# Optimization experiments

Hardware: AMD Instinct MI355X
Metric: run time of the kernel (lower is better)

## Reference

```python
import jax, jax.numpy as jnp
import numpy as np

H = 1024
T = 50000
WASHOUT = 200
SPECTRAL_RADIUS = 0.9


def setup_inputs() -> dict:
    key = jax.random.key(0)
    k_u, k_in, k_res, k_mask = jax.random.split(key, 4)
    u = jax.random.normal(k_u, (T,), dtype=jnp.float32)
    # w_in ~ Uniform(-0.5, 0.5), density 1.0, input_scaling 1.0
    w_in = jax.random.uniform(k_in, (H,), dtype=jnp.float32) - 0.5
    # w_res ~ Uniform(-0.5, 0.5), density 1.0, scaled to spectral radius 0.9
    w_res = np.asarray(jax.random.uniform(k_res, (H, H), dtype=jnp.float32)) - 0.5
    rho = float(np.max(np.abs(np.linalg.eigvals(w_res.astype(np.float64)))))
    w_res = jnp.asarray((SPECTRAL_RADIUS / rho) * w_res, dtype=jnp.float32)
    # readout weights (inference path uses the buffer, initialized to ones)
    w_out = jnp.ones((H,), dtype=jnp.float32)
    # w_out_density = 1.0 -> mask is a random permutation of all H indices
    w_out_mask = jax.random.permutation(k_mask, H).astype(jnp.int64)
    return {"u": u, "w_in": w_in, "w_res": w_res, "w_out": w_out,
            "w_out_mask": w_out_mask}


def reference(u, w_in, w_res, w_out, w_out_mask):
    # Echo-state recurrence: x_t = tanh(w_in * u_t + w_res @ x_{t-1})
    # Inference path (y=None, awgn_test_std=0, adc_quantization=None).
    def step(x, u_t):
        x_new = jnp.tanh(w_in * u_t + w_res @ x)  # [H]
        return x_new, x_new[w_out_mask]           # emit masked state

    x0 = jnp.zeros((H,), dtype=u.dtype)
    _, X = jax.lax.scan(step, x0, u)              # X: [T, H]
    return X[WASHOUT:] @ w_out                    # [T - WASHOUT]
```

## Files before the change

kernel.cpp:

```cpp
#include <hip/hip_runtime.h>


#define HH    1024
#define TT    50000
#define WASH  200
#define NBROLE 32
#define NBLK  512
#define NT    256
#define SPIN_CAP (1u << 20)
#define LDSPAD 98304

typedef unsigned int u32;
typedef u32 u32x4 __attribute__((ext_vector_type(4)));
typedef float f32x4 __attribute__((ext_vector_type(4)));
typedef float f32x2 __attribute__((ext_vector_type(2)));

__device__ __forceinline__ float fast_tanh(float x) {
  float e = __builtin_amdgcn_exp2f(x * 2.8853900817779268f);
  return fmaf(-2.0f, __builtin_amdgcn_rcpf(e + 1.0f), 1.0f);
}

template <int CTRL>
__device__ __forceinline__ float dpp_movf(float x) {
  return __int_as_float(__builtin_amdgcn_update_dpp(
      0, __float_as_int(x), CTRL, 0xF, 0xF, true));
}
__device__ __forceinline__ float swz_xor16(float x) {
  return __int_as_float(__builtin_amdgcn_ds_swizzle(__float_as_int(x), 0x401F));
}

#define YREDUCE()                                                         \
  { y += __shfl_xor(y, 32);                                               \
    y += swz_xor16(y);                                                    \
    y += dpp_movf<0x128>(y);                             \
    y += dpp_movf<0x141>(y);                             \
    y += dpp_movf<0x1B>(y);                              \
    y += dpp_movf<0xB1>(y); }

#define POLL_ISSUE1(b)                                                    \
  asm volatile("global_load_dwordx4 %0, %1, off sc1" : "=v"(p) : "v"(b))
#define POLL_WAIT1()                                                      \
  asm volatile("s_waitcnt vmcnt(0)" : "+v"(p))

#define TAGBAD(q) ((((q.x ^ want) | (q.y ^ want) | (q.z ^ want) | (q.w ^ want)) & 0xFFu))

#define UNPACK2(q, b2)                                                    \
  { xv2[b2+0] = (f32x2){__uint_as_float(q.x & 0xFFFFFF00u),               \
                        __uint_as_float(q.y & 0xFFFFFF00u)};              \
    xv2[b2+1] = (f32x2){__uint_as_float(q.z & 0xFFFFFF00u),               \
                        __uint_as_float(q.w & 0xFFFFFF00u)}; }

#define DECLW(r) f32x2 W##r##0, W##r##1, W##r##2, W##r##3,                \
                      W##r##4, W##r##5, W##r##6, W##r##7

#define LOADW(r) do {                                                     \
  const float* wp = w_res + (size_t)(32 * b + 8 * ww + r) * HH + 4 * l;   \
  f32x4 va = *(const f32x4*)(wp);                                         \
  f32x4 vb = *(const f32x4*)(wp + 256);                                   \
  f32x4 vc = *(const f32x4*)(wp + 512);                                   \
  f32x4 vd = *(const f32x4*)(wp + 768);                                   \
  W##r##0 = (f32x2){va.x, va.y}; W##r##1 = (f32x2){va.z, va.w};           \
  W##r##2 = (f32x2){vb.x, vb.y}; W##r##3 = (f32x2){vb.z, vb.w};           \
  W##r##4 = (f32x2){vc.x, vc.y}; W##r##5 = (f32x2){vc.z, vc.w};           \
  W##r##6 = (f32x2){vd.x, vd.y}; W##r##7 = (f32x2){vd.z, vd.w};           \
} while (0)

#define FMAR(r) do {                                                      \
  acc2[r] = __builtin_elementwise_fma(W##r##0, xv2[0], acc2[r]);          \
  acc2[r] = __builtin_elementwise_fma(W##r##1, xv2[1], acc2[r]);          \
  acc2[r] = __builtin_elementwise_fma(W##r##2, xv2[2], acc2[r]);          \
  acc2[r] = __builtin_elementwise_fma(W##r##3, xv2[3], acc2[r]);          \
  acc2[r] = __builtin_elementwise_fma(W##r##4, xv2[4], acc2[r]);          \
  acc2[r] = __builtin_elementwise_fma(W##r##5, xv2[5], acc2[r]);          \
  acc2[r] = __builtin_elementwise_fma(W##r##6, xv2[6], acc2[r]);          \
  acc2[r] = __builtin_elementwise_fma(W##r##7, xv2[7], acc2[r]);          \
} while (0)

__global__ __launch_bounds__(NT, 1) void esn_kernel(
    const float* __restrict__ u,
    const float* __restrict__ w_in,
    const float* __restrict__ w_res,
    const float* __restrict__ w_out,
    const int*   __restrict__ mask,
    float*       __restrict__ out,
    char*        __restrict__ ws)
{
  const int tid = threadIdx.x;
  const int l  = tid & 63;
  const int ww = tid >> 6;

  u32 xcc;
  asm("s_getreg_b32 %0, hwreg(HW_REG_XCC_ID)" : "=s"(xcc));
  if (xcc != 0) return;

  __shared__ __align__(16) char lds_all[LDSPAD];
  float* lds_c = (float*)lds_all;
  u32 (*lds_x)[HH] = (u32 (*)[HH])(lds_all + 4096);
  int* slot_p = (int*)(lds_all + 4096 + 8192);

  if (tid == 0) *slot_p = atomicAdd((int*)ws, 1);
  for (int h = tid; h < HH; h += NT) lds_c[mask[h]] = w_out[h];
  __syncthreads();
  const int b = *slot_p;
  if (b >= NBROLE) return;

  u32* xb0 = (u32*)(ws + 4096);
  u32* xb1 = xb0 + HH;

  DECLW(0); DECLW(1); DECLW(2); DECLW(3);
  DECLW(4); DECLW(5); DECLW(6); DECLW(7);
  LOADW(0); LOADW(1); LOADW(2); LOADW(3);
  LOADW(4); LOADW(5); LOADW(6); LOADW(7);

  const float win = w_in[32 * b + 8 * ww + (l >> 3)];

  f32x2 cr2[8];
#pragma unroll
  for (int k = 0; k < 4; ++k) {
    f32x4 v = *(const f32x4*)(lds_c + 256 * k + 4 * l);
    cr2[2*k+0] = (f32x2){v.x, v.y};
    cr2[2*k+1] = (f32x2){v.z, v.w};
  }

  const u32* pS0 = xb0 + 256 * ww + 4 * l;
  const u32* pS1 = xb1 + 256 * ww + 4 * l;
  const int drow = 32 * b + 8 * ww + (l >> 3);
  u32* d0 = xb0 + drow;
  u32* d1 = xb1 + drow;
  const int stg = 256 * ww + 4 * l;

  const int role = (b << 2) | ww;
  u32x4 p;
  const int lb32 = l & 32, lb16 = l & 16, lb8 = l & 8;
  int dead = 0;

  for (int t = 0; t < TT; ++t) {
    const int pa = t & 1;
    const float u_t = u[t];
    f32x2 acc2[8];
#pragma unroll
    for (int i = 0; i < 8; ++i) acc2[i] = (f32x2){0.f, 0.f};
    f32x2 xv2[8];
    const bool doRead = ((t & 127) == role) && (t > 0);

    if (t > 0) {
      const int h = pa ^ 1;
      if (!dead) {
        __builtin_amdgcn_s_sleep(2);
        const u32* src = h ? pS1 : pS0;
        const u32 want = (u32)t & 0xFFu;
        u32 guard = 0;
        for (;;) {
          POLL_ISSUE1(src);
          POLL_WAIT1();
          if (!TAGBAD(p)) break;
          if (++guard > SPIN_CAP) { dead = 1; break; }
        }
      }
      *(u32x4*)(&lds_x[h][stg]) = p;
      __syncthreads();
      u32x4 c0 = *(const u32x4*)(&lds_x[h][  0 + 4 * l]);
      u32x4 c1 = *(const u32x4*)(&lds_x[h][256 + 4 * l]);
      u32x4 c2 = *(const u32x4*)(&lds_x[h][512 + 4 * l]);
      u32x4 c3 = *(const u32x4*)(&lds_x[h][768 + 4 * l]);
      UNPACK2(c0, 0); UNPACK2(c1, 2); UNPACK2(c2, 4); UNPACK2(c3, 6);
      FMAR(0); FMAR(1); FMAR(2); FMAR(3);
      FMAR(4); FMAR(5); FMAR(6); FMAR(7);
    }

    const float a0 = acc2[0].x + acc2[0].y, a1 = acc2[1].x + acc2[1].y;
    const float a2 = acc2[2].x + acc2[2].y, a3 = acc2[3].x + acc2[3].y;
    const float a4 = acc2[4].x + acc2[4].y, a5 = acc2[5].x + acc2[5].y;
    const float a6 = acc2[6].x + acc2[6].y, a7 = acc2[7].x + acc2[7].y;
    float t0 = (lb32 ? a4 : a0) + __shfl_xor(lb32 ? a0 : a4, 32);
    float t1 = (lb32 ? a5 : a1) + __shfl_xor(lb32 ? a1 : a5, 32);
    float t2 = (lb32 ? a6 : a2) + __shfl_xor(lb32 ? a2 : a6, 32);
    float t3 = (lb32 ? a7 : a3) + __shfl_xor(lb32 ? a3 : a7, 32);
    float s0 = (lb16 ? t2 : t0) + swz_xor16(lb16 ? t0 : t2);
    float s1 = (lb16 ? t3 : t1) + swz_xor16(lb16 ? t1 : t3);
    float r0 = (lb8 ? s1 : s0) + dpp_movf<0x128>(lb8 ? s0 : s1);
    r0 += dpp_movf<0x141>(r0);
    r0 += dpp_movf<0x1B>(r0);
    r0 += dpp_movf<0xB1>(r0);

    float x_new = fast_tanh(fmaf(win, u_t, r0));
    u32 packed = ((__float_as_uint(x_new) + 0x80u) & 0xFFFFFF00u)
               | ((u32)(t + 1) & 0xFFu);
    if ((l & 7) == 0) {
      u32* dst = pa ? d1 : d0;
      asm volatile("global_store_dword %0, %1, off" :: "v"(dst), "v"(packed));
    }

    if (doRead) {
      f32x2 y2 = (f32x2){0.f, 0.f};
#pragma unroll
      for (int jj = 0; jj < 8; ++jj)
        y2 = __builtin_elementwise_fma(cr2[jj], xv2[jj], y2);
      float y = y2.x + y2.y;
      YREDUCE();
      if (l == 0 && t - 1 >= WASH) out[t - 1 - WASH] = y;
    }
  }

  if (b == 0) {
    const u32 want = (u32)TT & 0xFFu;
    u32 guard = 0;
    for (;;) {
      POLL_ISSUE1(pS1);
      POLL_WAIT1();
      if (!TAGBAD(p)) break;
      if (++guard > SPIN_CAP) break;
    }
    *(u32x4*)(&lds_x[1][stg]) = p;
    __syncthreads();
    if (ww == 0) {
      f32x2 xv2[8];
      u32x4 c0 = *(const u32x4*)(&lds_x[1][  0 + 4 * l]);
      u32x4 c1 = *(const u32x4*)(&lds_x[1][256 + 4 * l]);
      u32x4 c2 = *(const u32x4*)(&lds_x[1][512 + 4 * l]);
      u32x4 c3 = *(const u32x4*)(&lds_x[1][768 + 4 * l]);
      UNPACK2(c0, 0); UNPACK2(c1, 2); UNPACK2(c2, 4); UNPACK2(c3, 6);
      f32x2 y2 = (f32x2){0.f, 0.f};
#pragma unroll
      for (int jj = 0; jj < 8; ++jj)
        y2 = __builtin_elementwise_fma(cr2[jj], xv2[jj], y2);
      float y = y2.x + y2.y;
      YREDUCE();
      if (l == 0) out[TT - 1 - WASH] = y;
    }
  }
}

extern "C" void kernel_launch(void* const* d_in, const int* in_sizes, int n_in,
                              void* d_out, int out_size, void* d_ws, size_t ws_size,
                              hipStream_t stream) {
  const float* u     = (const float*)d_in[0];
  const float* w_in  = (const float*)d_in[1];
  const float* w_res = (const float*)d_in[2];
  const float* w_out = (const float*)d_in[3];
  const int*   mask  = (const int*)d_in[4];
  float* out = (float*)d_out;

  hipMemsetAsync(d_ws, 0, 64, stream);

  esn_kernel<<<NBLK, NT, 0, stream>>>(u, w_in, w_res, w_out, mask, out,
                                      (char*)d_ws);
}
```

Measured before the change: 42.10 ms.

## Replace block barrier with per-wave LDS flags and consume state quarters incrementally

Each wave now publishes its polled slice of the previous state to LDS and raises a per-wave tagged flag, instead of every wave meeting at a __syncthreads. Waves consume their own quarter at once from registers and spin on the other waves' flags one quarter at a time, interleaving FMAs with waiting. This aims to cut barrier latency on the serial recurrence's critical path and to overlap compute with late-arriving slices. The cost is LDS spin polling, and correctness relies on volatile LDS ordering and on the 8-bit time tags not aliasing.

```diff
diff --git a/kernel.cpp b/kernel.cpp
--- a/kernel.cpp
+++ b/kernel.cpp
@@ -65,15 +65,24 @@
   W##r##6 = (f32x2){vd.x, vd.y}; W##r##7 = (f32x2){vd.z, vd.w};           \
 } while (0)
 
-#define FMAR(r) do {                                                      \
-  acc2[r] = __builtin_elementwise_fma(W##r##0, xv2[0], acc2[r]);          \
-  acc2[r] = __builtin_elementwise_fma(W##r##1, xv2[1], acc2[r]);          \
-  acc2[r] = __builtin_elementwise_fma(W##r##2, xv2[2], acc2[r]);          \
-  acc2[r] = __builtin_elementwise_fma(W##r##3, xv2[3], acc2[r]);          \
-  acc2[r] = __builtin_elementwise_fma(W##r##4, xv2[4], acc2[r]);          \
-  acc2[r] = __builtin_elementwise_fma(W##r##5, xv2[5], acc2[r]);          \
-  acc2[r] = __builtin_elementwise_fma(W##r##6, xv2[6], acc2[r]);          \
-  acc2[r] = __builtin_elementwise_fma(W##r##7, xv2[7], acc2[r]);          \
+#define FMAQ(r, pA, pB)                                                   \
+  acc2[r] = __builtin_elementwise_fma(W##r##pA, xv2[pA], acc2[r]);        \
+  acc2[r] = __builtin_elementwise_fma(W##r##pB, xv2[pB], acc2[r]);
+#define FMAQALL(pA, pB)                                                   \
+  FMAQ(0, pA, pB) FMAQ(1, pA, pB) FMAQ(2, pA, pB) FMAQ(3, pA, pB)         \
+  FMAQ(4, pA, pB) FMAQ(5, pA, pB) FMAQ(6, pA, pB) FMAQ(7, pA, pB)
+
+#define QUARTER(q, pA, pB) do {                                           \
+  u32x4 cq;                                                               \
+  if (q == ww) { cq = p; }                                                \
+  else {                                                                  \
+    u32 g = 0;                                                            \
+    while (vflg[(h << 2) | q] != want) { if (++g > SPIN_CAP) break; }     \
+    asm volatile("" ::: "memory");                                        \
+    cq = *(const u32x4*)(&lds_x[h][256 * q + 4 * l]);                     \
+  }                                                                       \
+  UNPACK2(cq, 2 * q);                                                     \
+  FMAQALL(pA, pB);                                                        \
 } while (0)
 
 __global__ __launch_bounds__(NT, 1) void esn_kernel(
@@ -96,9 +105,11 @@
   __shared__ __align__(16) char lds_all[LDSPAD];
   float* lds_c = (float*)lds_all;
   u32 (*lds_x)[HH] = (u32 (*)[HH])(lds_all + 4096);
-  int* slot_p = (int*)(lds_all + 4096 + 8192);
+  volatile u32* vflg = (volatile u32*)(lds_all + 4096 + 8192);
+  int* slot_p = (int*)(lds_all + 4096 + 8192 + 32);
 
   if (tid == 0) *slot_p = atomicAdd((int*)ws, 1);
+  if (tid < 8) vflg[tid] = 0xAAAAAAAAu;
   for (int h = tid; h < HH; h += NT) lds_c[mask[h]] = w_out[h];
   __syncthreads();
   const int b = *slot_p;
@@ -145,10 +156,10 @@
 
     if (t > 0) {
       const int h = pa ^ 1;
+      const u32 want = (u32)t & 0xFFu;
       if (!dead) {
         __builtin_amdgcn_s_sleep(2);
         const u32* src = h ? pS1 : pS0;
-        const u32 want = (u32)t & 0xFFu;
         u32 guard = 0;
         for (;;) {
           POLL_ISSUE1(src);
@@ -158,14 +169,12 @@
         }
       }
       *(u32x4*)(&lds_x[h][stg]) = p;
-      __syncthreads();
-      u32x4 c0 = *(const u32x4*)(&lds_x[h][  0 + 4 * l]);
-      u32x4 c1 = *(const u32x4*)(&lds_x[h][256 + 4 * l]);
-      u32x4 c2 = *(const u32x4*)(&lds_x[h][512 + 4 * l]);
-      u32x4 c3 = *(const u32x4*)(&lds_x[h][768 + 4 * l]);
-      UNPACK2(c0, 0); UNPACK2(c1, 2); UNPACK2(c2, 4); UNPACK2(c3, 6);
-      FMAR(0); FMAR(1); FMAR(2); FMAR(3);
-      FMAR(4); FMAR(5); FMAR(6); FMAR(7);
+      asm volatile("s_waitcnt lgkmcnt(0)" ::: "memory");
+      vflg[(h << 2) | ww] = want;
+      QUARTER(0, 0, 1);
+      QUARTER(1, 2, 3);
+      QUARTER(2, 4, 5);
+      QUARTER(3, 6, 7);
     }
 
     const float a0 = acc2[0].x + acc2[0].y, a1 = acc2[1].x + acc2[1].y;
```

Result: slower. 54.39 ms (+29.2%).

## Poll full state vector per wave, removing LDS staging and block barrier

Applied to the files above, without the earlier changes.

Each wave now polls all four 1KB chunks of the previous state vector directly from global memory with four dwordx4 loads, instead of each wave polling one quarter and sharing through LDS behind a __syncthreads. This removes the per-step block barrier and the LDS round trip from the serial critical path. In exchange, global polling traffic per block rises fourfold, and each wave spins on its own, which may add contention on the shared buffer.

```diff
diff --git a/kernel.cpp b/kernel.cpp
--- a/kernel.cpp
+++ b/kernel.cpp
@@ -37,12 +37,17 @@
     y += dpp_movf<0x1B>(y);                              \
     y += dpp_movf<0xB1>(y); }
 
-#define POLL_ISSUE1(b)                                                    \
-  asm volatile("global_load_dwordx4 %0, %1, off sc1" : "=v"(p) : "v"(b))
-#define POLL_WAIT1()                                                      \
-  asm volatile("s_waitcnt vmcnt(0)" : "+v"(p))
+#define POLL_ISSUE4(bp)                                                               \
+  asm volatile("global_load_dwordx4 %0, %1, off sc1"             : "=v"(p0) : "v"(bp)); \
+  asm volatile("global_load_dwordx4 %0, %1, off offset:1024 sc1" : "=v"(p1) : "v"(bp)); \
+  asm volatile("global_load_dwordx4 %0, %1, off offset:2048 sc1" : "=v"(p2) : "v"(bp)); \
+  asm volatile("global_load_dwordx4 %0, %1, off offset:3072 sc1" : "=v"(p3) : "v"(bp))
+#define POLL_WAIT0()                                                      \
+  asm volatile("s_waitcnt vmcnt(0)"                                       \
+               : "+v"(p0), "+v"(p1), "+v"(p2), "+v"(p3))
 
 #define TAGBAD(q) ((((q.x ^ want) | (q.y ^ want) | (q.z ^ want) | (q.w ^ want)) & 0xFFu))
+#define TAGBAD_ALL (TAGBAD(p0) | TAGBAD(p1) | TAGBAD(p2) | TAGBAD(p3))
 
 #define UNPACK2(q, b2)                                                    \
   { xv2[b2+0] = (f32x2){__uint_as_float(q.x & 0xFFFFFF00u),               \
@@ -95,8 +100,7 @@
 
   __shared__ __align__(16) char lds_all[LDSPAD];
   float* lds_c = (float*)lds_all;
-  u32 (*lds_x)[HH] = (u32 (*)[HH])(lds_all + 4096);
-  int* slot_p = (int*)(lds_all + 4096 + 8192);
+  int* slot_p = (int*)(lds_all + 4096);
 
   if (tid == 0) *slot_p = atomicAdd((int*)ws, 1);
   for (int h = tid; h < HH; h += NT) lds_c[mask[h]] = w_out[h];
@@ -122,15 +126,14 @@
     cr2[2*k+1] = (f32x2){v.z, v.w};
   }
 
-  const u32* pS0 = xb0 + 256 * ww + 4 * l;
-  const u32* pS1 = xb1 + 256 * ww + 4 * l;
+  const u32* pA0 = xb0 + 4 * l;
+  const u32* pA1 = xb1 + 4 * l;
   const int drow = 32 * b + 8 * ww + (l >> 3);
   u32* d0 = xb0 + drow;
   u32* d1 = xb1 + drow;
-  const int stg = 256 * ww + 4 * l;
 
   const int role = (b << 2) | ww;
-  u32x4 p;
+  u32x4 p0, p1, p2, p3;
   const int lb32 = l & 32, lb16 = l & 16, lb8 = l & 8;
   int dead = 0;
 
@@ -144,26 +147,19 @@
     const bool doRead = ((t & 127) == role) && (t > 0);
 
     if (t > 0) {
-      const int h = pa ^ 1;
       if (!dead) {
         __builtin_amdgcn_s_sleep(2);
-        const u32* src = h ? pS1 : pS0;
+        const u32* src = pa ? pA0 : pA1;
         const u32 want = (u32)t & 0xFFu;
         u32 guard = 0;
         for (;;) {
-          POLL_ISSUE1(src);
-          POLL_WAIT1();
-          if (!TAGBAD(p)) break;
+          POLL_ISSUE4(src);
+          POLL_WAIT0();
+          if (!TAGBAD_ALL) break;
           if (++guard > SPIN_CAP) { dead = 1; break; }
         }
       }
-      *(u32x4*)(&lds_x[h][stg]) = p;
-      __syncthreads();
-      u32x4 c0 = *(const u32x4*)(&lds_x[h][  0 + 4 * l]);
-      u32x4 c1 = *(const u32x4*)(&lds_x[h][256 + 4 * l]);
-      u32x4 c2 = *(const u32x4*)(&lds_x[h][512 + 4 * l]);
-      u32x4 c3 = *(const u32x4*)(&lds_x[h][768 + 4 * l]);
-      UNPACK2(c0, 0); UNPACK2(c1, 2); UNPACK2(c2, 4); UNPACK2(c3, 6);
+      UNPACK2(p0, 0); UNPACK2(p1, 2); UNPACK2(p2, 4); UNPACK2(p3, 6);
       FMAR(0); FMAR(1); FMAR(2); FMAR(3);
       FMAR(4); FMAR(5); FMAR(6); FMAR(7);
     }
@@ -202,32 +198,24 @@
     }
   }
 
-  if (b == 0) {
+  if (b == 0 && ww == 0) {
     const u32 want = (u32)TT & 0xFFu;
     u32 guard = 0;
     for (;;) {
-      POLL_ISSUE1(pS1);
-      POLL_WAIT1();
-      if (!TAGBAD(p)) break;
+      POLL_ISSUE4(pA1);
+      POLL_WAIT0();
+      if (!TAGBAD_ALL) break;
       if (++guard > SPIN_CAP) break;
     }
-    *(u32x4*)(&lds_x[1][stg]) = p;
-    __syncthreads();
-    if (ww == 0) {
-      f32x2 xv2[8];
-      u32x4 c0 = *(const u32x4*)(&lds_x[1][  0 + 4 * l]);
-      u32x4 c1 = *(const u32x4*)(&lds_x[1][256 + 4 * l]);
-      u32x4 c2 = *(const u32x4*)(&lds_x[1][512 + 4 * l]);
-      u32x4 c3 = *(const u32x4*)(&lds_x[1][768 + 4 * l]);
-      UNPACK2(c0, 0); UNPACK2(c1, 2); UNPACK2(c2, 4); UNPACK2(c3, 6);
-      f32x2 y2 = (f32x2){0.f, 0.f};
-#pragma unroll
-      for (int jj = 0; jj < 8; ++jj)
-        y2 = __builtin_elementwise_fma(cr2[jj], xv2[jj], y2);
-      float y = y2.x + y2.y;
-      YREDUCE();
-      if (l == 0) out[TT - 1 - WASH] = y;
-    }
+    f32x2 xv2[8];
+    UNPACK2(p0, 0); UNPACK2(p1, 2); UNPACK2(p2, 4); UNPACK2(p3, 6);
+    f32x2 y2 = (f32x2){0.f, 0.f};
+#pragma unroll
+    for (int jj = 0; jj < 8; ++jj)
+      y2 = __builtin_elementwise_fma(cr2[jj], xv2[jj], y2);
+    float y = y2.x + y2.y;
+    YREDUCE();
+    if (l == 0) out[TT - 1 - WASH] = y;
   }
 }
 
```

Measured after the change: 42.83 ms. Within noise of the previous version (+1.7%).

## Move readout dot product to a dedicated fifth wavefront off the recurrence path

Applied to the files above, without the earlier changes.

Each block gets a fifth wavefront (256 to 320 threads). In block 0 this wave polls the published state itself and computes the masked readout for every timestep. In other blocks it only matches the per-step __syncthreads. This takes the rotating per-step readout reduction out of the recurrence wavefronts' critical path. The cost is an extra wave per block that must hit every barrier, plus extra global polling traffic on the state buffer from block 0.

```diff
diff --git a/kernel.cpp b/kernel.cpp
--- a/kernel.cpp
+++ b/kernel.cpp
@@ -6,7 +6,7 @@
 #define WASH  200
 #define NBROLE 32
 #define NBLK  512
-#define NT    256
+#define NT    320
 #define SPIN_CAP (1u << 20)
 #define LDSPAD 98304
 
@@ -37,10 +37,19 @@
     y += dpp_movf<0x1B>(y);                              \
     y += dpp_movf<0xB1>(y); }
 
-#define POLL_ISSUE1(b)                                                    \
-  asm volatile("global_load_dwordx4 %0, %1, off sc1" : "=v"(p) : "v"(b))
+#define POLL_ISSUE1(bp)                                                   \
+  asm volatile("global_load_dwordx4 %0, %1, off sc1" : "=v"(p) : "v"(bp))
 #define POLL_WAIT1()                                                      \
   asm volatile("s_waitcnt vmcnt(0)" : "+v"(p))
+
+#define RISSUE(bp)                                                                    \
+  asm volatile("global_load_dwordx4 %0, %1, off sc1"             : "=v"(p0) : "v"(bp)); \
+  asm volatile("global_load_dwordx4 %0, %1, off offset:1024 sc1" : "=v"(p1) : "v"(bp)); \
+  asm volatile("global_load_dwordx4 %0, %1, off offset:2048 sc1" : "=v"(p2) : "v"(bp)); \
+  asm volatile("global_load_dwordx4 %0, %1, off offset:3072 sc1" : "=v"(p3) : "v"(bp))
+#define RWAIT()                                                           \
+  asm volatile("s_waitcnt vmcnt(0)"                                       \
+               : "+v"(p0), "+v"(p1), "+v"(p2), "+v"(p3))
 
 #define TAGBAD(q) ((((q.x ^ want) | (q.y ^ want) | (q.z ^ want) | (q.w ^ want)) & 0xFFu))
 
@@ -107,20 +116,77 @@
   u32* xb0 = (u32*)(ws + 4096);
   u32* xb1 = xb0 + HH;
 
+  if (ww == 4) {
+    if (b != 0) {
+      for (int t = 1; t < TT; ++t) __syncthreads();
+      return;
+    }
+    f32x2 cr2[8];
+#pragma unroll
+    for (int k = 0; k < 4; ++k) {
+      f32x4 v = *(const f32x4*)(lds_c + 256 * k + 4 * l);
+      cr2[2*k+0] = (f32x2){v.x, v.y};
+      cr2[2*k+1] = (f32x2){v.z, v.w};
+    }
+    const u32* rA0 = xb0 + 4 * l;
+    const u32* rA1 = xb1 + 4 * l;
+    u32x4 p0, p1, p2, p3;
+    int dead = 0;
+    for (int t = 1; t < TT; ++t) {
+      const bool work = (t - 1 >= WASH) && !dead;
+      if (work) {
+        __builtin_amdgcn_s_sleep(2);
+        const u32* src = ((t - 1) & 1) ? rA1 : rA0;
+        const u32 want = (u32)t & 0xFFu;
+        u32 guard = 0;
+        for (;;) {
+          RISSUE(src);
+          RWAIT();
+          if (!(TAGBAD(p0) | TAGBAD(p1) | TAGBAD(p2) | TAGBAD(p3))) break;
+          if (++guard > SPIN_CAP) { dead = 1; break; }
+        }
+      }
+      __syncthreads();
+      if (work) {
+        f32x2 xv2[8];
+        UNPACK2(p0, 0); UNPACK2(p1, 2); UNPACK2(p2, 4); UNPACK2(p3, 6);
+        f32x2 y2 = (f32x2){0.f, 0.f};
+#pragma unroll
+        for (int jj = 0; jj < 8; ++jj)
+          y2 = __builtin_elementwise_fma(cr2[jj], xv2[jj], y2);
+        float y = y2.x + y2.y;
+        YREDUCE();
+        if (l == 0) out[t - 1 - WASH] = y;
+      }
+    }
+    if (!dead) {
+      const u32 want = (u32)TT & 0xFFu;
+      u32 guard = 0;
+      for (;;) {
+        RISSUE(rA1);
+        RWAIT();
+        if (!(TAGBAD(p0) | TAGBAD(p1) | TAGBAD(p2) | TAGBAD(p3))) break;
+        if (++guard > SPIN_CAP) break;
+      }
+      f32x2 xv2[8];
+      UNPACK2(p0, 0); UNPACK2(p1, 2); UNPACK2(p2, 4); UNPACK2(p3, 6);
+      f32x2 y2 = (f32x2){0.f, 0.f};
+#pragma unroll
+      for (int jj = 0; jj < 8; ++jj)
+        y2 = __builtin_elementwise_fma(cr2[jj], xv2[jj], y2);
+      float y = y2.x + y2.y;
+      YREDUCE();
+      if (l == 0) out[TT - 1 - WASH] = y;
+    }
+    return;
+  }
+
   DECLW(0); DECLW(1); DECLW(2); DECLW(3);
   DECLW(4); DECLW(5); DECLW(6); DECLW(7);
   LOADW(0); LOADW(1); LOADW(2); LOADW(3);
   LOADW(4); LOADW(5); LOADW(6); LOADW(7);
 
   const float win = w_in[32 * b + 8 * ww + (l >> 3)];
-
-  f32x2 cr2[8];
-#pragma unroll
-  for (int k = 0; k < 4; ++k) {
-    f32x4 v = *(const f32x4*)(lds_c + 256 * k + 4 * l);
-    cr2[2*k+0] = (f32x2){v.x, v.y};
-    cr2[2*k+1] = (f32x2){v.z, v.w};
-  }
 
   const u32* pS0 = xb0 + 256 * ww + 4 * l;
   const u32* pS1 = xb1 + 256 * ww + 4 * l;
@@ -129,7 +195,6 @@
   u32* d1 = xb1 + drow;
   const int stg = 256 * ww + 4 * l;
 
-  const int role = (b << 2) | ww;
   u32x4 p;
   const int lb32 = l & 32, lb16 = l & 16, lb8 = l & 8;
   int dead = 0;
@@ -141,7 +206,6 @@
 #pragma unroll
     for (int i = 0; i < 8; ++i) acc2[i] = (f32x2){0.f, 0.f};
     f32x2 xv2[8];
-    const bool doRead = ((t & 127) == role) && (t > 0);
 
     if (t > 0) {
       const int h = pa ^ 1;
@@ -190,44 +254,6 @@
       u32* dst = pa ? d1 : d0;
       asm volatile("global_store_dword %0, %1, off" :: "v"(dst), "v"(packed));
     }
-
-    if (doRead) {
-      f32x2 y2 = (f32x2){0.f, 0.f};
-#pragma unroll
-      for (int jj = 0; jj < 8; ++jj)
-        y2 = __builtin_elementwise_fma(cr2[jj], xv2[jj], y2);
-      float y = y2.x + y2.y;
-      YREDUCE();
-      if (l == 0 && t - 1 >= WASH) out[t - 1 - WASH] = y;
-    }
-  }
-
-  if (b == 0) {
-    const u32 want = (u32)TT & 0xFFu;
-    u32 guard = 0;
-    for (;;) {
-      POLL_ISSUE1(pS1);
-      POLL_WAIT1();
-      if (!TAGBAD(p)) break;
-      if (++guard > SPIN_CAP) break;
-    }
-    *(u32x4*)(&lds_x[1][stg]) = p;
-    __syncthreads();
-    if (ww == 0) {
-      f32x2 xv2[8];
-      u32x4 c0 = *(const u32x4*)(&lds_x[1][  0 + 4 * l]);
-      u32x4 c1 = *(const u32x4*)(&lds_x[1][256 + 4 * l]);
-      u32x4 c2 = *(const u32x4*)(&lds_x[1][512 + 4 * l]);
-      u32x4 c3 = *(const u32x4*)(&lds_x[1][768 + 4 * l]);
-      UNPACK2(c0, 0); UNPACK2(c1, 2); UNPACK2(c2, 4); UNPACK2(c3, 6);
-      f32x2 y2 = (f32x2){0.f, 0.f};
-#pragma unroll
-      for (int jj = 0; jj < 8; ++jj)
-        y2 = __builtin_elementwise_fma(cr2[jj], xv2[jj], y2);
-      float y = y2.x + y2.y;
-      YREDUCE();
-      if (l == 0) out[TT - 1 - WASH] = y;
-    }
   }
 }
 
```

Measured after the change: 41.84 ms. Within noise of the previous version (-0.6%).
